# Kernel optimization log

Hardware: AMD Instinct MI355X
Metric: run time of the kernel (lower is better)

## Reference

```python
import jax, jax.numpy as jnp
import numpy as np

D_MODEL = 1024
N_HEADS = 16
D_K = D_MODEL // N_HEADS  # 64
D_V = D_MODEL // N_HEADS  # 64
B, S = 2, 2048


def setup_inputs() -> dict:
    key = jax.random.key(0)
    ks = jax.random.split(key, 8)
    inp = {
        "Q": jax.random.normal(ks[0], (B, S, D_MODEL), dtype=jnp.float32),
        "K": jax.random.normal(ks[1], (B, S, D_MODEL), dtype=jnp.float32),
        "V": jax.random.normal(ks[2], (B, S, D_MODEL), dtype=jnp.float32),
        "prev": jax.random.normal(ks[3], (B, N_HEADS, S, S), dtype=jnp.float32) * 0.1,
        # torch nn.Linear weights are [out_features, in_features]
        "W_Q": jax.random.normal(ks[4], (N_HEADS * D_K, D_MODEL), dtype=jnp.float32) / np.sqrt(D_MODEL),
        "W_K": jax.random.normal(ks[5], (N_HEADS * D_K, D_MODEL), dtype=jnp.float32) / np.sqrt(D_MODEL),
        "W_V": jax.random.normal(ks[6], (N_HEADS * D_V, D_MODEL), dtype=jnp.float32) / np.sqrt(D_MODEL),
        "W_O": jax.random.normal(ks[7], (D_MODEL, N_HEADS * D_V), dtype=jnp.float32) / np.sqrt(N_HEADS * D_V),
    }
    return inp


def reference(Q, K, V, prev, W_Q, W_K, W_V, W_O):
    scale = D_K ** (-0.5)
    # projections: x @ W.T, then split heads -> (b, h, s, d)
    q = jnp.einsum('bsm,em->bse', Q, W_Q).reshape(B, S, N_HEADS, D_K).transpose(0, 2, 1, 3)
    k = jnp.einsum('bsm,em->bse', K, W_K).reshape(B, S, N_HEADS, D_K).transpose(0, 2, 1, 3)
    v = jnp.einsum('bsm,em->bse', V, W_V).reshape(B, S, N_HEADS, D_V).transpose(0, 2, 1, 3)
    scores = jnp.einsum('bhqd,bhkd->bhqk', q, k) * scale + prev
    attn = jax.nn.softmax(scores, axis=-1)  # attn_dropout = 0 (eval)
    context = jnp.einsum('bhqk,bhkd->bhqd', attn, v)
    context = context.transpose(0, 2, 1, 3).reshape(B, S, N_HEADS * D_V)
    output = jnp.einsum('bse,me->bsm', context, W_O)  # proj_dropout = 0 (eval)
    return (output, attn, scores)
```

## Files before the change

### kernel.cpp

```cpp
#include <hip/hip_runtime.h>

#define S_LEN 2048
#define NH 16
#define DH 64
#define DM 1024
#define NB 2
#define BS 4096

typedef __attribute__((ext_vector_type(4))) float f32x4;
typedef __attribute__((ext_vector_type(8))) short bfrag;

__device__ __forceinline__ unsigned short f2bf(float f) {
    unsigned u = __builtin_bit_cast(unsigned, f);
    u += 0x7FFFu + ((u >> 16) & 1u);
    return (unsigned short)(u >> 16);
}

__device__ __forceinline__ void gld16(const unsigned short* g, unsigned short* l) {
    __builtin_amdgcn_global_load_lds((const __attribute__((address_space(1))) void*)g,
                                     (__attribute__((address_space(3))) void*)l, 16, 0, 0);
}

__global__ __launch_bounds__(256) void cast_all(const float* __restrict__ Q,
                                                const float* __restrict__ K,
                                                const float* __restrict__ V,
                                                const float* __restrict__ Wq,
                                                const float* __restrict__ Wk,
                                                const float* __restrict__ Wv,
                                                const float* __restrict__ Wo,
                                                unsigned short* __restrict__ Qc,
                                                unsigned short* __restrict__ Kc,
                                                unsigned short* __restrict__ Vc,
                                                unsigned short* __restrict__ Wqc,
                                                unsigned short* __restrict__ Wkc,
                                                unsigned short* __restrict__ Wvc,
                                                unsigned short* __restrict__ Woc) {
    int i = blockIdx.x * 256 + threadIdx.x;
    const float* src;
    unsigned short* dst;
    int off;
    if (i < 3145728) {
        int w = i >> 20;
        off = i & 1048575;
        src = (w == 0) ? Q : (w == 1) ? K : V;
        dst = (w == 0) ? Qc : (w == 1) ? Kc : Vc;
    } else {
        int j = i - 3145728;
        int w = j >> 18;
        off = j & 262143;
        src = (w == 0) ? Wq : (w == 1) ? Wk : (w == 2) ? Wv : Wo;
        dst = (w == 0) ? Wqc : (w == 1) ? Wkc : (w == 2) ? Wvc : Woc;
    }
    float4 v = reinterpret_cast<const float4*>(src)[off];
    ushort4 o;
    o.x = f2bf(v.x); o.y = f2bf(v.y); o.z = f2bf(v.z); o.w = f2bf(v.w);
    reinterpret_cast<ushort4*>(dst)[off] = o;
}

__global__ __launch_bounds__(256) void gemm_qkv(const unsigned short* __restrict__ Qc,
                                                const unsigned short* __restrict__ Kc,
                                                const unsigned short* __restrict__ Vc,
                                                const unsigned short* __restrict__ Wqc,
                                                const unsigned short* __restrict__ Wkc,
                                                const unsigned short* __restrict__ Wvc,
                                                unsigned short* __restrict__ qh,
                                                unsigned short* __restrict__ kh,
                                                unsigned short* __restrict__ vT) {
    const int z = blockIdx.z;
    const unsigned short* A = (z == 0) ? Qc : (z == 1) ? Kc : Vc;
    const unsigned short* B = (z == 0) ? Wqc : (z == 1) ? Wkc : Wvc;
    const int tid = threadIdx.x, lane = tid & 63;
    const int l15 = lane & 15, lhi = lane >> 4;
    const int w = tid >> 6, wr = w >> 1, wc = w & 1;
    const int m0 = blockIdx.y * 128, n0 = blockIdx.x * 128;
    const int K = DM;
    const int lr8 = lane >> 3;
    const int csw = (lane & 7) ^ lr8;

    __shared__ unsigned short sA[128 * 64];
    __shared__ unsigned short sB[128 * 64];

    f32x4 acc[4][4];
#pragma unroll
    for (int i = 0; i < 4; ++i)
#pragma unroll
        for (int j = 0; j < 4; ++j) acc[i][j] = (f32x4){0.f, 0.f, 0.f, 0.f};

    for (int t = 0; t < 16; ++t) {
        const int k0 = t * 64;
#pragma unroll
        for (int i = 0; i < 4; ++i) {
            int g = w * 4 + i;
            int row = g * 8 + lr8;
            gld16(A + (size_t)(m0 + row) * K + k0 + csw * 8, sA + g * 512);
            gld16(B + (size_t)(n0 + row) * K + k0 + csw * 8, sB + g * 512);
        }
        __syncthreads();
#pragma unroll
        for (int kk = 0; kk < 2; ++kk) {
            bfrag a[4], b[4];
#pragma unroll
            for (int f = 0; f < 4; ++f) {
                int ra = wr * 64 + f * 16 + l15;
                a[f] = *reinterpret_cast<const bfrag*>(
                    sA + ra * 64 + (((kk * 4 + lhi) ^ (ra & 7)) << 3));
                int rb = wc * 64 + f * 16 + l15;
                b[f] = *reinterpret_cast<const bfrag*>(
                    sB + rb * 64 + (((kk * 4 + lhi) ^ (rb & 7)) << 3));
            }
#pragma unroll
            for (int fm = 0; fm < 4; ++fm)
#pragma unroll
                for (int fn = 0; fn < 4; ++fn)
                    acc[fm][fn] =
                        __builtin_amdgcn_mfma_f32_16x16x32_bf16(a[fm], b[fn], acc[fm][fn], 0, 0, 0);
        }
        __syncthreads();
    }

    if (z == 2) {
#pragma unroll
        for (int fm = 0; fm < 4; ++fm)
#pragma unroll
            for (int fn = 0; fn < 4; ++fn) {
                int sbase = m0 + wr * 64 + fm * 16 + (lhi << 2);
                int gcol = n0 + wc * 64 + fn * 16 + l15;
                int b = sbase >> 11, s = sbase & 2047, h = gcol >> 6, d = gcol & 63;
                ushort4 o;
                o.x = f2bf(acc[fm][fn][0]); o.y = f2bf(acc[fm][fn][1]);
                o.z = f2bf(acc[fm][fn][2]); o.w = f2bf(acc[fm][fn][3]);
                *reinterpret_cast<ushort4*>(vT + ((size_t)(b * NH + h) * DH + d) * S_LEN + s) = o;
            }
    } else {
        unsigned short* Out = (z == 0) ? qh : kh;
#pragma unroll
        for (int fm = 0; fm < 4; ++fm)
#pragma unroll
            for (int fn = 0; fn < 4; ++fn)
#pragma unroll
                for (int r = 0; r < 4; ++r) {
                    int grow = m0 + wr * 64 + fm * 16 + (lhi << 2) + r;
                    int gcol = n0 + wc * 64 + fn * 16 + l15;
                    int b = grow >> 11, s = grow & 2047, h = gcol >> 6, d = gcol & 63;
                    Out[((size_t)(b * NH + h) * S_LEN + s) * DH + d] = f2bf(acc[fm][fn][r]);
                }
    }
}

__global__ __launch_bounds__(256) void gemm_out(const unsigned short* __restrict__ A,
                                                const unsigned short* __restrict__ B,
                                                float* __restrict__ Out) {
    const int tid = threadIdx.x, lane = tid & 63;
    const int l15 = lane & 15, lhi = lane >> 4;
    const int w = tid >> 6, wr = w >> 1, wc = w & 1;
    const int m0 = blockIdx.y * 128, n0 = blockIdx.x * 128;
    const int K = DM, N = DM;
    const int lr8 = lane >> 3;
    const int csw = (lane & 7) ^ lr8;

    __shared__ unsigned short sA[128 * 64];
    __shared__ unsigned short sB[128 * 64];

    f32x4 acc[4][4];
#pragma unroll
    for (int i = 0; i < 4; ++i)
#pragma unroll
        for (int j = 0; j < 4; ++j) acc[i][j] = (f32x4){0.f, 0.f, 0.f, 0.f};

    for (int t = 0; t < 16; ++t) {
        const int k0 = t * 64;
#pragma unroll
        for (int i = 0; i < 4; ++i) {
            int g = w * 4 + i;
            int row = g * 8 + lr8;
            gld16(A + (size_t)(m0 + row) * K + k0 + csw * 8, sA + g * 512);
            gld16(B + (size_t)(n0 + row) * K + k0 + csw * 8, sB + g * 512);
        }
        __syncthreads();
#pragma unroll
        for (int kk = 0; kk < 2; ++kk) {
            bfrag a[4], b[4];
#pragma unroll
            for (int f = 0; f < 4; ++f) {
                int ra = wr * 64 + f * 16 + l15;
                a[f] = *reinterpret_cast<const bfrag*>(
                    sA + ra * 64 + (((kk * 4 + lhi) ^ (ra & 7)) << 3));
                int rb = wc * 64 + f * 16 + l15;
                b[f] = *reinterpret_cast<const bfrag*>(
                    sB + rb * 64 + (((kk * 4 + lhi) ^ (rb & 7)) << 3));
            }
#pragma unroll
            for (int fm = 0; fm < 4; ++fm)
#pragma unroll
                for (int fn = 0; fn < 4; ++fn)
                    acc[fm][fn] =
                        __builtin_amdgcn_mfma_f32_16x16x32_bf16(a[fm], b[fn], acc[fm][fn], 0, 0, 0);
        }
        __syncthreads();
    }

#pragma unroll
    for (int fm = 0; fm < 4; ++fm)
#pragma unroll
        for (int fn = 0; fn < 4; ++fn)
#pragma unroll
            for (int r = 0; r < 4; ++r) {
                int grow = m0 + wr * 64 + fm * 16 + (lhi << 2) + r;
                int gcol = n0 + wc * 64 + fn * 16 + l15;
                Out[(size_t)grow * N + gcol] = acc[fm][fn][r];
            }
}

__global__ __launch_bounds__(64, 4) void attn_fused(const unsigned short* __restrict__ qh,
                                                    const unsigned short* __restrict__ kh,
                                                    const unsigned short* __restrict__ vT,
                                                    const float* __restrict__ prev,
                                                    float* __restrict__ scores,
                                                    float* __restrict__ attn,
                                                    unsigned short* __restrict__ ctx) {
    const int z = blockIdx.z;
    const int m0 = blockIdx.x * 16;
    const int lane = threadIdx.x & 63;
    const int l15 = lane & 15, lhi = lane >> 4;

    const unsigned short* Qz = qh + (size_t)z * S_LEN * DH;
    const unsigned short* Kz = kh + (size_t)z * S_LEN * DH;
    const unsigned short* Vz = vT + (size_t)z * DH * S_LEN;
    const size_t zbase = (size_t)z * S_LEN * S_LEN;
    const float scale = 0.125f;

    const int qrow = l15;
    const float* prevRow = prev + zbase + (size_t)(m0 + qrow) * S_LEN;
    float* scoresRow = scores + zbase + (size_t)(m0 + qrow) * S_LEN;
    float* attnRow = attn + zbase + (size_t)(m0 + qrow) * S_LEN;
    const int c4 = lhi * 4;
    const int c8 = lhi * 8;

    bfrag qf[2];
#pragma unroll
    for (int kk = 0; kk < 2; ++kk)
        qf[kk] = *reinterpret_cast<const bfrag*>(Qz + (size_t)(m0 + qrow) * DH + kk * 32 +
                                                 lhi * 8);

    float m_r = -1e30f, l_r = 0.f;

    bfrag kf[2][4];
#pragma unroll
    for (int kk = 0; kk < 2; ++kk)
#pragma unroll
        for (int f = 0; f < 4; ++f)
            kf[kk][f] = *reinterpret_cast<const bfrag*>(
                Kz + (size_t)(f * 16 + l15) * DH + kk * 32 + lhi * 8);
    f32x4 pv4[4];
#pragma unroll
    for (int f = 0; f < 4; ++f)
        pv4[f] = __builtin_nontemporal_load(
            reinterpret_cast<const f32x4*>(prevRow + f * 16 + c4));

    for (int kt = 0; kt < 32; ++kt) {
        const int n0 = kt * 64;

        f32x4 acc[4];
#pragma unroll
        for (int f = 0; f < 4; ++f) acc[f] = (f32x4){0.f, 0.f, 0.f, 0.f};
#pragma unroll
        for (int kk = 0; kk < 2; ++kk)
#pragma unroll
            for (int f = 0; f < 4; ++f)
                acc[f] = __builtin_amdgcn_mfma_f32_16x16x32_bf16(kf[kk][f], qf[kk], acc[f], 0, 0, 0);

        if (kt < 31) {
            const int n1 = n0 + 64;
#pragma unroll
            for (int kk = 0; kk < 2; ++kk)
#pragma unroll
                for (int f = 0; f < 4; ++f)
                    kf[kk][f] = *reinterpret_cast<const bfrag*>(
                        Kz + (size_t)(n1 + f * 16 + l15) * DH + kk * 32 + lhi * 8);
        }

#pragma unroll
        for (int f = 0; f < 4; ++f)
#pragma unroll
            for (int r = 0; r < 4; ++r) acc[f][r] = acc[f][r] * scale + pv4[f][r];
        if (kt < 31) {
            const int n1 = n0 + 64;
#pragma unroll
            for (int f = 0; f < 4; ++f)
                pv4[f] = __builtin_nontemporal_load(
                    reinterpret_cast<const f32x4*>(prevRow + n1 + f * 16 + c4));
        }
#pragma unroll
        for (int f = 0; f < 4; ++f)
            *reinterpret_cast<f32x4*>(scoresRow + n0 + f * 16 + c4) = acc[f];

        float pm = acc[0][0];
#pragma unroll
        for (int f = 0; f < 4; ++f)
#pragma unroll
            for (int r = 0; r < 4; ++r) pm = fmaxf(pm, acc[f][r]);
        pm = fmaxf(pm, __shfl_xor(pm, 16));
        pm = fmaxf(pm, __shfl_xor(pm, 32));
        float mnew = fmaxf(m_r, pm);
        float psum = 0.f;
#pragma unroll
        for (int f = 0; f < 4; ++f)
#pragma unroll
            for (int r = 0; r < 4; ++r) psum += __expf(acc[f][r] - mnew);
        psum += __shfl_xor(psum, 16);
        psum += __shfl_xor(psum, 32);
        l_r = l_r * __expf(m_r - mnew) + psum;
        m_r = mnew;
    }

    const float inv_l = 1.0f / l_r;

    f32x4 acco[4];
#pragma unroll
    for (int f = 0; f < 4; ++f) acco[f] = (f32x4){0.f, 0.f, 0.f, 0.f};

    bfrag vf[2][4];
#pragma unroll
    for (int kk = 0; kk < 2; ++kk)
#pragma unroll
        for (int f = 0; f < 4; ++f)
            vf[kk][f] = *reinterpret_cast<const bfrag*>(
                Vz + (size_t)(f * 16 + l15) * S_LEN + 31 * 64 + kk * 32 + lhi * 8);
    f32x4 sv[2][2];
#pragma unroll
    for (int kk = 0; kk < 2; ++kk)
#pragma unroll
        for (int h = 0; h < 2; ++h)
            sv[kk][h] = *reinterpret_cast<const f32x4*>(scoresRow + 31 * 64 + kk * 32 + c8 + h * 4);

    for (int kt = 31; kt >= 0; --kt) {
        const int n0 = kt * 64;
        bfrag pf[2];
#pragma unroll
        for (int kk = 0; kk < 2; ++kk) {
#pragma unroll
            for (int h = 0; h < 2; ++h) {
                f32x4 p4;
#pragma unroll
                for (int r = 0; r < 4; ++r) p4[r] = __expf(sv[kk][h][r] - m_r) * inv_l;
                __builtin_nontemporal_store(
                    p4, reinterpret_cast<f32x4*>(attnRow + n0 + kk * 32 + c8 + h * 4));
#pragma unroll
                for (int r = 0; r < 4; ++r) pf[kk][h * 4 + r] = (short)f2bf(p4[r]);
            }
        }
        if (kt > 0) {
            const int n1 = n0 - 64;
#pragma unroll
            for (int kk = 0; kk < 2; ++kk)
#pragma unroll
                for (int h = 0; h < 2; ++h)
                    sv[kk][h] =
                        *reinterpret_cast<const f32x4*>(scoresRow + n1 + kk * 32 + c8 + h * 4);
        }
#pragma unroll
        for (int kk = 0; kk < 2; ++kk)
#pragma unroll
            for (int f = 0; f < 4; ++f)
                acco[f] = __builtin_amdgcn_mfma_f32_16x16x32_bf16(vf[kk][f], pf[kk], acco[f], 0, 0, 0);
        if (kt > 0) {
            const int n1 = n0 - 64;
#pragma unroll
            for (int kk = 0; kk < 2; ++kk)
#pragma unroll
                for (int f = 0; f < 4; ++f)
                    vf[kk][f] = *reinterpret_cast<const bfrag*>(
                        Vz + (size_t)(f * 16 + l15) * S_LEN + n1 + kk * 32 + lhi * 8);
        }
    }

    const int b = z >> 4, h = z & 15;
    const int s = m0 + qrow;
#pragma unroll
    for (int f = 0; f < 4; ++f) {
        int d0 = f * 16 + c4;
        ushort4 o;
        o.x = f2bf(acco[f][0]); o.y = f2bf(acco[f][1]);
        o.z = f2bf(acco[f][2]); o.w = f2bf(acco[f][3]);
        *reinterpret_cast<ushort4*>(ctx + ((size_t)(b * S_LEN + s)) * DM + h * DH + d0) = o;
    }
}

extern "C" void kernel_launch(void* const* d_in, const int* in_sizes, int n_in, void* d_out,
                              int out_size, void* d_ws, size_t ws_size, hipStream_t stream) {
    const float* Q = (const float*)d_in[0];
    const float* K = (const float*)d_in[1];
    const float* V = (const float*)d_in[2];
    const float* prev = (const float*)d_in[3];
    const float* Wq = (const float*)d_in[4];
    const float* Wk = (const float*)d_in[5];
    const float* Wv = (const float*)d_in[6];
    const float* Wo = (const float*)d_in[7];

    float* out = (float*)d_out;
    float* attn = out + (size_t)BS * DM;
    float* scores = attn + (size_t)NB * NH * S_LEN * S_LEN;

    unsigned short* ws = (unsigned short*)d_ws;
    unsigned short* Qc = ws;
    unsigned short* Kc = Qc + (size_t)BS * DM;
    unsigned short* Vc = Kc + (size_t)BS * DM;
    unsigned short* Wqc = Vc + (size_t)BS * DM;
    unsigned short* Wkc = Wqc + (size_t)DM * DM;
    unsigned short* Wvc = Wkc + (size_t)DM * DM;
    unsigned short* Woc = Wvc + (size_t)DM * DM;
    unsigned short* qh = Woc + (size_t)DM * DM;
    unsigned short* kh = qh + (size_t)BS * DM;
    unsigned short* vT = kh + (size_t)BS * DM;
    unsigned short* ctx = vT + (size_t)BS * DM;

    cast_all<<<16384, 256, 0, stream>>>(Q, K, V, Wq, Wk, Wv, Wo,
                                        Qc, Kc, Vc, Wqc, Wkc, Wvc, Woc);

    dim3 gq(DM / 128, BS / 128, 3);
    gemm_qkv<<<gq, 256, 0, stream>>>(Qc, Kc, Vc, Wqc, Wkc, Wvc, qh, kh, vT);

    dim3 ga(S_LEN / 16, 1, NB * NH);
    attn_fused<<<ga, 64, 0, stream>>>(qh, kh, vT, prev, scores, attn, ctx);

    dim3 gp(DM / 128, BS / 128, 1);
    gemm_out<<<gp, 256, 0, stream>>>(ctx, Woc, out);
}
```

Before: 724.9 us.

## Transpose score tiles through LDS for row-contiguous prev/scores/attn access

After: 631.4 us. -12.9%, faster.

```diff
diff --git a/kernel.cpp b/kernel.cpp
--- a/kernel.cpp
+++ b/kernel.cpp
@@ -19,6 +19,11 @@
 __device__ __forceinline__ void gld16(const unsigned short* g, unsigned short* l) {
     __builtin_amdgcn_global_load_lds((const __attribute__((address_space(1))) void*)g,
                                      (__attribute__((address_space(3))) void*)l, 16, 0, 0);
+}
+
+__device__ __forceinline__ void lds_fence() {
+    asm volatile("s_waitcnt lgkmcnt(0)" ::: "memory");
+    __builtin_amdgcn_sched_barrier(0);
 }
 
 __global__ __launch_bounds__(256) void cast_all(const float* __restrict__ Q,
@@ -211,7 +216,7 @@
             }
 }
 
-__global__ __launch_bounds__(64, 4) void attn_fused(const unsigned short* __restrict__ qh,
+__global__ __launch_bounds__(64, 3) void attn_fused(const unsigned short* __restrict__ qh,
                                                     const unsigned short* __restrict__ kh,
                                                     const unsigned short* __restrict__ vT,
                                                     const float* __restrict__ prev,
@@ -222,6 +227,11 @@
     const int m0 = blockIdx.x * 16;
     const int lane = threadIdx.x & 63;
     const int l15 = lane & 15, lhi = lane >> 4;
+    const int crow = lane >> 4;
+    const int ccol = (lane & 15) * 4;
+
+    __shared__ float sT[16 * 64];
+    unsigned short* sB = reinterpret_cast<unsigned short*>(sT);
 
     const unsigned short* Qz = qh + (size_t)z * S_LEN * DH;
     const unsigned short* Kz = kh + (size_t)z * S_LEN * DH;
@@ -229,20 +239,20 @@
     const size_t zbase = (size_t)z * S_LEN * S_LEN;
     const float scale = 0.125f;
 
-    const int qrow = l15;
-    const float* prevRow = prev + zbase + (size_t)(m0 + qrow) * S_LEN;
-    float* scoresRow = scores + zbase + (size_t)(m0 + qrow) * S_LEN;
-    float* attnRow = attn + zbase + (size_t)(m0 + qrow) * S_LEN;
-    const int c4 = lhi * 4;
-    const int c8 = lhi * 8;
+    size_t ro[4];
+#pragma unroll
+    for (int i = 0; i < 4; ++i)
+        ro[i] = zbase + (size_t)(m0 + i * 4 + crow) * S_LEN + ccol;
 
     bfrag qf[2];
 #pragma unroll
     for (int kk = 0; kk < 2; ++kk)
-        qf[kk] = *reinterpret_cast<const bfrag*>(Qz + (size_t)(m0 + qrow) * DH + kk * 32 +
+        qf[kk] = *reinterpret_cast<const bfrag*>(Qz + (size_t)(m0 + l15) * DH + kk * 32 +
                                                  lhi * 8);
 
-    float m_r = -1e30f, l_r = 0.f;
+    float m_r[4], l_r[4];
+#pragma unroll
+    for (int i = 0; i < 4; ++i) { m_r[i] = -1e30f; l_r[i] = 0.f; }
 
     bfrag kf[2][4];
 #pragma unroll
@@ -253,9 +263,8 @@
                 Kz + (size_t)(f * 16 + l15) * DH + kk * 32 + lhi * 8);
     f32x4 pv4[4];
 #pragma unroll
-    for (int f = 0; f < 4; ++f)
-        pv4[f] = __builtin_nontemporal_load(
-            reinterpret_cast<const f32x4*>(prevRow + f * 16 + c4));
+    for (int i = 0; i < 4; ++i)
+        pv4[i] = __builtin_nontemporal_load(reinterpret_cast<const f32x4*>(prev + ro[i]));
 
     for (int kt = 0; kt < 32; ++kt) {
         const int n0 = kt * 64;
@@ -281,39 +290,52 @@
 
 #pragma unroll
         for (int f = 0; f < 4; ++f)
-#pragma unroll
-            for (int r = 0; r < 4; ++r) acc[f][r] = acc[f][r] * scale + pv4[f][r];
+            *reinterpret_cast<f32x4*>(sT + l15 * 64 + (((f * 4 + lhi) ^ (l15 & 7)) * 4)) = acc[f];
+        lds_fence();
+        f32x4 sc[4];
+#pragma unroll
+        for (int i = 0; i < 4; ++i) {
+            int r = i * 4 + crow;
+            sc[i] = *reinterpret_cast<const f32x4*>(sT + r * 64 + ((l15 ^ (r & 7)) * 4));
+        }
+
+#pragma unroll
+        for (int i = 0; i < 4; ++i)
+#pragma unroll
+            for (int r = 0; r < 4; ++r) sc[i][r] = sc[i][r] * scale + pv4[i][r];
         if (kt < 31) {
             const int n1 = n0 + 64;
 #pragma unroll
-            for (int f = 0; f < 4; ++f)
-                pv4[f] = __builtin_nontemporal_load(
-                    reinterpret_cast<const f32x4*>(prevRow + n1 + f * 16 + c4));
-        }
-#pragma unroll
-        for (int f = 0; f < 4; ++f)
-            *reinterpret_cast<f32x4*>(scoresRow + n0 + f * 16 + c4) = acc[f];
-
-        float pm = acc[0][0];
-#pragma unroll
-        for (int f = 0; f < 4; ++f)
-#pragma unroll
-            for (int r = 0; r < 4; ++r) pm = fmaxf(pm, acc[f][r]);
-        pm = fmaxf(pm, __shfl_xor(pm, 16));
-        pm = fmaxf(pm, __shfl_xor(pm, 32));
-        float mnew = fmaxf(m_r, pm);
-        float psum = 0.f;
-#pragma unroll
-        for (int f = 0; f < 4; ++f)
-#pragma unroll
-            for (int r = 0; r < 4; ++r) psum += __expf(acc[f][r] - mnew);
-        psum += __shfl_xor(psum, 16);
-        psum += __shfl_xor(psum, 32);
-        l_r = l_r * __expf(m_r - mnew) + psum;
-        m_r = mnew;
-    }
-
-    const float inv_l = 1.0f / l_r;
+            for (int i = 0; i < 4; ++i)
+                pv4[i] = __builtin_nontemporal_load(
+                    reinterpret_cast<const f32x4*>(prev + ro[i] + n1));
+        }
+#pragma unroll
+        for (int i = 0; i < 4; ++i)
+            *reinterpret_cast<f32x4*>(scores + ro[i] + n0) = sc[i];
+
+#pragma unroll
+        for (int i = 0; i < 4; ++i) {
+            float pm = fmaxf(fmaxf(sc[i][0], sc[i][1]), fmaxf(sc[i][2], sc[i][3]));
+            pm = fmaxf(pm, __shfl_xor(pm, 1));
+            pm = fmaxf(pm, __shfl_xor(pm, 2));
+            pm = fmaxf(pm, __shfl_xor(pm, 4));
+            pm = fmaxf(pm, __shfl_xor(pm, 8));
+            float mnew = fmaxf(m_r[i], pm);
+            float ps = __expf(sc[i][0] - mnew) + __expf(sc[i][1] - mnew) +
+                       __expf(sc[i][2] - mnew) + __expf(sc[i][3] - mnew);
+            ps += __shfl_xor(ps, 1);
+            ps += __shfl_xor(ps, 2);
+            ps += __shfl_xor(ps, 4);
+            ps += __shfl_xor(ps, 8);
+            l_r[i] = l_r[i] * __expf(m_r[i] - mnew) + ps;
+            m_r[i] = mnew;
+        }
+    }
+
+    float inv_l[4];
+#pragma unroll
+    for (int i = 0; i < 4; ++i) inv_l[i] = 1.0f / l_r[i];
 
     f32x4 acco[4];
 #pragma unroll
@@ -326,37 +348,42 @@
         for (int f = 0; f < 4; ++f)
             vf[kk][f] = *reinterpret_cast<const bfrag*>(
                 Vz + (size_t)(f * 16 + l15) * S_LEN + 31 * 64 + kk * 32 + lhi * 8);
-    f32x4 sv[2][2];
-#pragma unroll
-    for (int kk = 0; kk < 2; ++kk)
-#pragma unroll
-        for (int h = 0; h < 2; ++h)
-            sv[kk][h] = *reinterpret_cast<const f32x4*>(scoresRow + 31 * 64 + kk * 32 + c8 + h * 4);
+    f32x4 sv[4];
+#pragma unroll
+    for (int i = 0; i < 4; ++i)
+        sv[i] = *reinterpret_cast<const f32x4*>(scores + ro[i] + 31 * 64);
 
     for (int kt = 31; kt >= 0; --kt) {
         const int n0 = kt * 64;
+#pragma unroll
+        for (int i = 0; i < 4; ++i) {
+            int r = i * 4 + crow;
+            f32x4 p4;
+#pragma unroll
+            for (int rr = 0; rr < 4; ++rr) p4[rr] = __expf(sv[i][rr] - m_r[i]) * inv_l[i];
+            __builtin_nontemporal_store(p4, reinterpret_cast<f32x4*>(attn + ro[i] + n0));
+            ushort4 pb;
+            pb.x = f2bf(p4[0]); pb.y = f2bf(p4[1]); pb.z = f2bf(p4[2]); pb.w = f2bf(p4[3]);
+            *reinterpret_cast<ushort4*>(sB + r * 64 + ((l15 ^ (r & 7)) * 4)) = pb;
+        }
+        lds_fence();
         bfrag pf[2];
 #pragma unroll
         for (int kk = 0; kk < 2; ++kk) {
-#pragma unroll
-            for (int h = 0; h < 2; ++h) {
-                f32x4 p4;
-#pragma unroll
-                for (int r = 0; r < 4; ++r) p4[r] = __expf(sv[kk][h][r] - m_r) * inv_l;
-                __builtin_nontemporal_store(
-                    p4, reinterpret_cast<f32x4*>(attnRow + n0 + kk * 32 + c8 + h * 4));
-#pragma unroll
-                for (int r = 0; r < 4; ++r) pf[kk][h * 4 + r] = (short)f2bf(p4[r]);
-            }
+            int c0 = kk * 8 + lhi * 2;
+            ushort4 lo = *reinterpret_cast<const ushort4*>(sB + l15 * 64 + ((c0 ^ (l15 & 7)) * 4));
+            ushort4 hi =
+                *reinterpret_cast<const ushort4*>(sB + l15 * 64 + (((c0 + 1) ^ (l15 & 7)) * 4));
+            pf[kk][0] = (short)lo.x; pf[kk][1] = (short)lo.y;
+            pf[kk][2] = (short)lo.z; pf[kk][3] = (short)lo.w;
+            pf[kk][4] = (short)hi.x; pf[kk][5] = (short)hi.y;
+            pf[kk][6] = (short)hi.z; pf[kk][7] = (short)hi.w;
         }
         if (kt > 0) {
             const int n1 = n0 - 64;
 #pragma unroll
-            for (int kk = 0; kk < 2; ++kk)
-#pragma unroll
-                for (int h = 0; h < 2; ++h)
-                    sv[kk][h] =
-                        *reinterpret_cast<const f32x4*>(scoresRow + n1 + kk * 32 + c8 + h * 4);
+            for (int i = 0; i < 4; ++i)
+                sv[i] = *reinterpret_cast<const f32x4*>(scores + ro[i] + n1);
         }
 #pragma unroll
         for (int kk = 0; kk < 2; ++kk)
@@ -375,10 +402,10 @@
     }
 
     const int b = z >> 4, h = z & 15;
-    const int s = m0 + qrow;
+    const int s = m0 + l15;
 #pragma unroll
     for (int f = 0; f < 4; ++f) {
-        int d0 = f * 16 + c4;
+        int d0 = f * 16 + lhi * 4;
         ushort4 o;
         o.x = f2bf(acco[f][0]); o.y = f2bf(acco[f][1]);
         o.z = f2bf(acco[f][2]); o.w = f2bf(acco[f][3]);
```
